# Kernel tuning notes

Measured on AMD Instinct MI355X. Metric: run time of the kernel, lower is better.

The kernel has to match this reference:

```python
import jax, jax.numpy as jnp
import numpy as np

EPS = 1e-8


def setup_inputs() -> dict:
    key = jax.random.key(0)
    k1, k2 = jax.random.split(key)
    x = jax.random.normal(k1, (32, 16, 4096), dtype=jnp.float32)
    # shapelets param: (in_channels, num_shapelets, shapelets_size)
    shapelets = jax.random.normal(k2, (16, 64, 64), dtype=jnp.float32)
    return {"x": x, "shapelets": shapelets}


def reference(x, shapelets):
    # x: (B, C, L); shapelets: (C, K, S)
    S = shapelets.shape[2]
    C = x.shape[1]
    W = x.shape[2] - S + 1
    # sliding windows, equivalent to torch unfold(2, S, 1): (B, C, W, S)
    idx = jnp.arange(W)[:, None] + jnp.arange(S)[None, :]
    win = x[:, :, idx]
    win = win / jnp.maximum(jnp.linalg.norm(win, axis=3, keepdims=True), EPS)
    sh = shapelets / jnp.maximum(jnp.linalg.norm(shapelets, axis=2, keepdims=True), EPS)
    # pairwise cosine dot, then mean over channels: (B, W, K)
    sim = jnp.einsum('bcws,cks->bwk', win, sh) / C
    # relu then global max over window positions; torch keeps the summed dim -> (B, 1, K)
    out = jnp.max(jax.nn.relu(sim), axis=1)[:, None, :]
    return out
```

## Files before the change

kernel.cpp:

```cpp
#include <hip/hip_runtime.h>

typedef unsigned int u32;
typedef unsigned short u16;
typedef __bf16 bf16x8 __attribute__((ext_vector_type(8)));
typedef float f32x4 __attribute__((ext_vector_type(4)));

static __device__ __forceinline__ u16 f2bf(float f) {
  u32 u = __float_as_uint(f);
  return (u16)((u + 0x7fffu + ((u >> 16) & 1u)) >> 16);
}
static __device__ __forceinline__ u32 pk2(u16 lo, u16 hi) {
  return (u32)lo | ((u32)hi << 16);
}

__global__ __launch_bounds__(256) void prep_kernel(const float* __restrict__ sh,
                                                   u16* __restrict__ shn2,
                                                   float* __restrict__ out) {
  if (blockIdx.x == 0) {
    float4 z = {0.f, 0.f, 0.f, 0.f};
    *(float4*)&out[threadIdx.x * 8] = z;
    *(float4*)&out[threadIdx.x * 8 + 4] = z;
  }
  const int s = threadIdx.x & 63;
  const int wv = threadIdx.x >> 6;
  const int row0 = blockIdx.x * 16 + wv * 4;
#pragma unroll
  for (int r = 0; r < 4; ++r) {
    const int row = row0 + r;
    float v = sh[row * 64 + s];
    float ss = v * v;
#pragma unroll
    for (int o = 1; o < 64; o <<= 1) ss += __shfl_xor(ss, o, 64);
    float iw = 1.0f / fmaxf(sqrtf(ss), 1e-8f);
    const int c = row >> 6, k = row & 63;
    const int chunk = c * 8 + (k >> 4) * 2 + (s >> 5);
    const int pos = ((k & 15) + (((s & 31) >> 3) << 4)) * 8 + (s & 7);
    shn2[chunk * 512 + pos] = f2bf(v * iw);
  }
}

#define WT 256
#define CSTRIDE 168
#define SSTRIDE 2728

__global__ __launch_bounds__(512, 2) void main_kernel(const float* __restrict__ x,
                                                      const u16* __restrict__ shn2,
                                                      float* __restrict__ out) {
  __shared__ u32 xs[4 * SSTRIDE];
  __shared__ float invwb[16 * WT];
  __shared__ int redbuf[64];

  const int tid = threadIdx.x;
  const int lane = tid & 63;
  const int wid = tid >> 6;
  const int w0 = blockIdx.x * WT;
  const int b = blockIdx.y;
  const float* xb = x + (size_t)b * 16 * 4096;

  if (tid < 64) redbuf[tid] = 0;

  {
    const int q = tid & 31;
    const int c = tid >> 5;
    if (q < 20) {
      const float* xc = xb + c * 4096;
      const int e0 = w0 + 16 * q;
      float xv[20];
      if (e0 + 19 < 4096) {
#pragma unroll
        for (int r = 0; r < 5; ++r) *(float4*)&xv[4 * r] = *(const float4*)&xc[e0 + 4 * r];
      } else {
#pragma unroll
        for (int j = 0; j < 20; ++j) {
          int g = e0 + j;
          xv[j] = xc[g < 4096 ? g : 4095];
        }
      }
      u16 bf[20];
#pragma unroll
      for (int j = 0; j < 20; ++j) bf[j] = f2bf(xv[j]);
#pragma unroll
      for (int s = 0; s < 4; ++s) {
        u32 pk[8];
#pragma unroll
        for (int r = 0; r < 8; ++r) pk[r] = pk2(bf[2 * r + s], bf[2 * r + s + 1]);
        u32* dst = &xs[s * SSTRIDE + c * CSTRIDE + 8 * q];
        *(uint4*)dst = make_uint4(pk[0], pk[1], pk[2], pk[3]);
        *(uint4*)(dst + 4) = make_uint4(pk[4], pk[5], pk[6], pk[7]);
      }
    }
  }

  {
    const int c = tid >> 5;
    const int wb = (tid & 31) * 8;
    const float* xc = xb + c * 4096;
    const int e0 = w0 + wb;
    float hd[8], tl[8], ss = 0.f;
    if (e0 + 71 < 4096) {
#pragma unroll
      for (int r = 0; r < 16; ++r) {
        float4 v = *(const float4*)&xc[e0 + 4 * r];
        if (r < 2) {
          hd[4 * r + 0] = v.x; hd[4 * r + 1] = v.y;
          hd[4 * r + 2] = v.z; hd[4 * r + 3] = v.w;
        }
        ss += v.x * v.x + v.y * v.y + v.z * v.z + v.w * v.w;
      }
#pragma unroll
      for (int r = 0; r < 2; ++r) {
        float4 v = *(const float4*)&xc[e0 + 64 + 4 * r];
        tl[4 * r + 0] = v.x; tl[4 * r + 1] = v.y;
        tl[4 * r + 2] = v.z; tl[4 * r + 3] = v.w;
      }
    } else {
#pragma unroll
      for (int j = 0; j < 72; ++j) {
        int g = e0 + j;
        float v = xc[g < 4096 ? g : 4095];
        if (j < 8) hd[j] = v;
        if (j >= 64) tl[j - 64] = v;
        if (j < 64) ss += v * v;
      }
    }
    float ov[8];
#pragma unroll
    for (int i = 0; i < 8; ++i) {
      float iw = 0.0625f / fmaxf(sqrtf(fmaxf(ss, 0.f)), 1e-8f);
      ov[i] = (e0 + i < 4033) ? iw : 0.f;
      ss += tl[i] * tl[i] - hd[i] * hd[i];
    }
    *(float4*)&invwb[c * WT + wb] = make_float4(ov[0], ov[1], ov[2], ov[3]);
    *(float4*)&invwb[c * WT + wb + 4] = make_float4(ov[4], ov[5], ov[6], ov[7]);
  }

  __syncthreads();

  f32x4 acc[4][2];
#pragma unroll
  for (int mt = 0; mt < 4; ++mt)
#pragma unroll
    for (int nt = 0; nt < 2; ++nt) acc[mt][nt] = (f32x4){0.f, 0.f, 0.f, 0.f};

  const int m = lane & 15;
  const int h = lane >> 4;
  const int wgrp = wid >> 1;
  const int kgrp = wid & 1;
  const u32* xbase = xs + (m & 3) * SSTRIDE;
  const int joff = 32 * wgrp + 2 * (m >> 2) + 4 * h;
  const u16* shb = shn2 + lane * 8 + kgrp * 4 * 512;
  const int iwbase = 64 * wgrp + 4 * h;

#pragma unroll 2
  for (int c = 0; c < 16; ++c) {
    const u32* xc = xbase + c * CSTRIDE;
    bf16x8 af[6];
#pragma unroll
    for (int f = 0; f < 6; ++f) {
      const u32* p = xc + joff + 8 * f;
      uint2 lo = *(const uint2*)p;
      uint2 hi = *(const uint2*)(p + 2);
      af[f] = __builtin_bit_cast(bf16x8, make_uint4(lo.x, lo.y, hi.x, hi.y));
    }
    const u16* sc = shb + c * 4096;
    bf16x8 bfr[2][2];
#pragma unroll
    for (int nt = 0; nt < 2; ++nt)
#pragma unroll
      for (int ks = 0; ks < 2; ++ks)
        bfr[nt][ks] = __builtin_bit_cast(bf16x8, *(const uint4*)(sc + (nt * 2 + ks) * 512));

#pragma unroll
    for (int mt = 0; mt < 4; ++mt) {
      f32x4 iw = *(const f32x4*)&invwb[c * WT + iwbase + 16 * mt];
#pragma unroll
      for (int nt = 0; nt < 2; ++nt) {
        f32x4 d = {0.f, 0.f, 0.f, 0.f};
        d = __builtin_amdgcn_mfma_f32_16x16x32_bf16(af[mt],     bfr[nt][0], d, 0, 0, 0);
        d = __builtin_amdgcn_mfma_f32_16x16x32_bf16(af[mt + 2], bfr[nt][1], d, 0, 0, 0);
        acc[mt][nt] += iw * d;
      }
    }
  }

#pragma unroll
  for (int nt = 0; nt < 2; ++nt) {
    float v = 0.f;
#pragma unroll
    for (int mt = 0; mt < 4; ++mt)
      v = fmaxf(v, fmaxf(fmaxf(acc[mt][nt].x, acc[mt][nt].y),
                         fmaxf(acc[mt][nt].z, acc[mt][nt].w)));
    v = fmaxf(v, __shfl_xor(v, 16, 64));
    v = fmaxf(v, __shfl_xor(v, 32, 64));
    if (lane < 16) atomicMax(&redbuf[kgrp * 32 + nt * 16 + lane], __float_as_int(v));
  }
  __syncthreads();
  if (tid < 64) atomicMax((int*)&out[b * 64 + tid], redbuf[tid]);
}

extern "C" void kernel_launch(void* const* d_in, const int* in_sizes, int n_in,
                              void* d_out, int out_size, void* d_ws, size_t ws_size,
                              hipStream_t stream) {
  const float* x = (const float*)d_in[0];
  const float* sh = (const float*)d_in[1];
  float* out = (float*)d_out;
  u16* shn2 = (u16*)d_ws;

  prep_kernel<<<dim3(64), dim3(256), 0, stream>>>(sh, shn2, out);
  main_kernel<<<dim3(16, 32), dim3(512), 0, stream>>>(x, shn2, out);
}
```

Baseline: 37.18 us.

## Swap MFMA operand roles so shapelets are A and windows are B

```diff
diff --git a/kernel.cpp b/kernel.cpp
--- a/kernel.cpp
+++ b/kernel.cpp
@@ -42,12 +42,13 @@
 #define WT 256
 #define CSTRIDE 168
 #define SSTRIDE 2728
+#define IWS 264
 
 __global__ __launch_bounds__(512, 2) void main_kernel(const float* __restrict__ x,
                                                       const u16* __restrict__ shn2,
                                                       float* __restrict__ out) {
   __shared__ u32 xs[4 * SSTRIDE];
-  __shared__ float invwb[16 * WT];
+  __shared__ float invwb[16 * IWS];
   __shared__ int redbuf[64];
 
   const int tid = threadIdx.x;
@@ -130,69 +131,70 @@
       ov[i] = (e0 + i < 4033) ? iw : 0.f;
       ss += tl[i] * tl[i] - hd[i] * hd[i];
     }
-    *(float4*)&invwb[c * WT + wb] = make_float4(ov[0], ov[1], ov[2], ov[3]);
-    *(float4*)&invwb[c * WT + wb + 4] = make_float4(ov[4], ov[5], ov[6], ov[7]);
+    *(float4*)&invwb[c * IWS + wb] = make_float4(ov[0], ov[1], ov[2], ov[3]);
+    *(float4*)&invwb[c * IWS + wb + 4] = make_float4(ov[4], ov[5], ov[6], ov[7]);
   }
 
   __syncthreads();
 
   f32x4 acc[4][2];
 #pragma unroll
-  for (int mt = 0; mt < 4; ++mt)
-#pragma unroll
-    for (int nt = 0; nt < 2; ++nt) acc[mt][nt] = (f32x4){0.f, 0.f, 0.f, 0.f};
+  for (int kt = 0; kt < 4; ++kt)
+#pragma unroll
+    for (int wt = 0; wt < 2; ++wt) acc[kt][wt] = (f32x4){0.f, 0.f, 0.f, 0.f};
 
   const int m = lane & 15;
   const int h = lane >> 4;
-  const int wgrp = wid >> 1;
-  const int kgrp = wid & 1;
   const u32* xbase = xs + (m & 3) * SSTRIDE;
-  const int joff = 32 * wgrp + 2 * (m >> 2) + 4 * h;
-  const u16* shb = shn2 + lane * 8 + kgrp * 4 * 512;
-  const int iwbase = 64 * wgrp + 4 * h;
+  const int joff = 16 * wid + 2 * (m >> 2) + 4 * h;
+  const u16* shb = shn2 + lane * 8;
+  const int iwoff = 32 * wid + m;
 
 #pragma unroll 2
   for (int c = 0; c < 16; ++c) {
     const u32* xc = xbase + c * CSTRIDE;
-    bf16x8 af[6];
-#pragma unroll
-    for (int f = 0; f < 6; ++f) {
-      const u32* p = xc + joff + 8 * f;
-      uint2 lo = *(const uint2*)p;
-      uint2 hi = *(const uint2*)(p + 2);
-      af[f] = __builtin_bit_cast(bf16x8, make_uint4(lo.x, lo.y, hi.x, hi.y));
-    }
+    bf16x8 bw[2][2];
+#pragma unroll
+    for (int wt = 0; wt < 2; ++wt)
+#pragma unroll
+      for (int ks = 0; ks < 2; ++ks) {
+        const u32* p = xc + joff + 8 * wt + 16 * ks;
+        uint2 lo = *(const uint2*)p;
+        uint2 hi = *(const uint2*)(p + 2);
+        bw[wt][ks] = __builtin_bit_cast(bf16x8, make_uint4(lo.x, lo.y, hi.x, hi.y));
+      }
+    float iw0 = invwb[c * IWS + iwoff];
+    float iw1 = invwb[c * IWS + iwoff + 16];
     const u16* sc = shb + c * 4096;
-    bf16x8 bfr[2][2];
-#pragma unroll
-    for (int nt = 0; nt < 2; ++nt)
-#pragma unroll
-      for (int ks = 0; ks < 2; ++ks)
-        bfr[nt][ks] = __builtin_bit_cast(bf16x8, *(const uint4*)(sc + (nt * 2 + ks) * 512));
-
-#pragma unroll
-    for (int mt = 0; mt < 4; ++mt) {
-      f32x4 iw = *(const f32x4*)&invwb[c * WT + iwbase + 16 * mt];
-#pragma unroll
-      for (int nt = 0; nt < 2; ++nt) {
-        f32x4 d = {0.f, 0.f, 0.f, 0.f};
-        d = __builtin_amdgcn_mfma_f32_16x16x32_bf16(af[mt],     bfr[nt][0], d, 0, 0, 0);
-        d = __builtin_amdgcn_mfma_f32_16x16x32_bf16(af[mt + 2], bfr[nt][1], d, 0, 0, 0);
-        acc[mt][nt] += iw * d;
-      }
-    }
-  }
-
-#pragma unroll
-  for (int nt = 0; nt < 2; ++nt) {
-    float v = 0.f;
-#pragma unroll
-    for (int mt = 0; mt < 4; ++mt)
-      v = fmaxf(v, fmaxf(fmaxf(acc[mt][nt].x, acc[mt][nt].y),
-                         fmaxf(acc[mt][nt].z, acc[mt][nt].w)));
-    v = fmaxf(v, __shfl_xor(v, 16, 64));
-    v = fmaxf(v, __shfl_xor(v, 32, 64));
-    if (lane < 16) atomicMax(&redbuf[kgrp * 32 + nt * 16 + lane], __float_as_int(v));
+#pragma unroll
+    for (int kt = 0; kt < 4; ++kt) {
+      bf16x8 a0 = __builtin_bit_cast(bf16x8, *(const uint4*)(sc + (kt * 2 + 0) * 512));
+      bf16x8 a1 = __builtin_bit_cast(bf16x8, *(const uint4*)(sc + (kt * 2 + 1) * 512));
+      f32x4 d0 = {0.f, 0.f, 0.f, 0.f}, d1 = {0.f, 0.f, 0.f, 0.f};
+      d0 = __builtin_amdgcn_mfma_f32_16x16x32_bf16(a0, bw[0][0], d0, 0, 0, 0);
+      d0 = __builtin_amdgcn_mfma_f32_16x16x32_bf16(a1, bw[0][1], d0, 0, 0, 0);
+      d1 = __builtin_amdgcn_mfma_f32_16x16x32_bf16(a0, bw[1][0], d1, 0, 0, 0);
+      d1 = __builtin_amdgcn_mfma_f32_16x16x32_bf16(a1, bw[1][1], d1, 0, 0, 0);
+      acc[kt][0] += iw0 * d0;
+      acc[kt][1] += iw1 * d1;
+    }
+  }
+
+#pragma unroll
+  for (int kt = 0; kt < 4; ++kt) {
+    f32x4 v4;
+#pragma unroll
+    for (int j = 0; j < 4; ++j)
+      v4[j] = fmaxf(fmaxf(acc[kt][0][j], acc[kt][1][j]), 0.f);
+#pragma unroll
+    for (int o = 1; o < 16; o <<= 1)
+#pragma unroll
+      for (int j = 0; j < 4; ++j) v4[j] = fmaxf(v4[j], __shfl_xor(v4[j], o, 64));
+    if (m == 0) {
+#pragma unroll
+      for (int j = 0; j < 4; ++j)
+        atomicMax(&redbuf[kt * 16 + 4 * h + j], __float_as_int(v4[j]));
+    }
   }
   __syncthreads();
   if (tid < 64) atomicMax((int*)&out[b * 64 + tid], redbuf[tid]);
```

Result: slower. 40.68 us (+9.4%).
